# Performance work log

Measured on AMD Instinct MI355X. Metric: run time of the kernel, lower is better.

## Reference

```python
import jax, jax.numpy as jnp
import numpy as np

N = 65536          # nodes per snapshot
B = 32             # batch
COMP = 2           # components (u, v)
SFC = 2            # number of space-filling-curve orderings
K, S, P = 32, 4, 16  # dimension==2 branch: kernel, stride, padding
CHANNELS = [2, 4, 8, 16, 16, 16]  # per-layer channels (x2 until num_final_channels=16)
NCONV = 5          # conv sizes: 65536->16385->4097->1025->257->65
FINAL_SIZE = 65


def _neigh_idx(n):
    # get_neighbourhood_md(arange(n), gen_neighbour_keys(1), ordering=True):
    # per-node [i-1, i, i+1], clamped at boundaries.
    i = jnp.arange(n)
    return jnp.stack([jnp.clip(i - 1, 0, n - 1), i, jnp.clip(i + 1, 0, n - 1)], axis=-1)


def setup_inputs() -> dict:
    key = jax.random.key(0)
    ks = jax.random.split(key, 16)
    d = {}
    d["x"] = jax.random.normal(ks[0], (B, N, COMP), jnp.float32)
    d["orderings"] = jax.random.randint(ks[1], (SFC, N), 0, N)  # SFC permutations (gather indices)
    d["sp_w"] = jnp.ones((N, 3), jnp.float32) / 3.0  # NearestNeighbouring weights (shared over sfcs)
    d["sp_b"] = jnp.zeros((N,), jnp.float32)
    for j in range(NCONV):
        cin, cout = CHANNELS[j], CHANNELS[j + 1]
        d[f"conv_w{j}"] = jax.random.normal(ks[2 + j], (cout, cin, K), jnp.float32) * (1.0 / np.sqrt(cin * K))
        d[f"conv_b{j}"] = jnp.zeros((cout,), jnp.float32)
    fc_in = SFC * CHANNELS[-1] * FINAL_SIZE  # 2080
    d["fc1_w"] = jax.random.normal(ks[8], (128, fc_in), jnp.float32) * (1.0 / np.sqrt(fc_in))
    d["fc1_b"] = jnp.zeros((128,), jnp.float32)
    d["fc2_w"] = jax.random.normal(ks[9], (16, 128), jnp.float32) * (1.0 / np.sqrt(128))
    d["fc2_b"] = jnp.zeros((16,), jnp.float32)
    return d


def _forward(x, orderings, sp_w, sp_b, conv_ws, conv_bs, fc1_w, fc1_b, fc2_w, fc2_b):
    neigh = _neigh_idx(N)  # (N,3)
    feats = []
    for i in range(SFC):
        a = x[:, orderings[i], :]            # SFC permutation gather -> (B,N,C)
        a = jnp.transpose(a, (0, 2, 1))      # (B,C,N)
        g = a[:, :, neigh]                   # neighbourhood gather -> (B,C,N,3)
        a = jnp.tanh(jnp.einsum('bcnk,nk->bcn', g, sp_w) + sp_b)  # sparse NN combine
        for w, b in zip(conv_ws, conv_bs):
            a = jax.lax.conv_general_dilated(a, w, (S,), [(P, P)],
                                             dimension_numbers=('NCH', 'OIH', 'NCH'))
            a = jnp.tanh(a + b[None, :, None])
        feats.append(a.reshape(a.shape[0], -1))  # (B, 16*65)
    h = jnp.concatenate(feats, axis=-1)          # (B, 2080)
    h = jnp.tanh(h @ fc1_w.T + fc1_b)            # (B, 128)
    h = jnp.tanh(h @ fc2_w.T + fc2_b)            # (B, 16) latent
    return h


def reference(x, orderings, sp_w, sp_b, conv_w0, conv_b0, conv_w1, conv_b1, conv_w2, conv_b2,
              conv_w3, conv_b3, conv_w4, conv_b4, fc1_w, fc1_b, fc2_w, fc2_b):
    conv_ws = [conv_w0, conv_w1, conv_w2, conv_w3, conv_w4]
    conv_bs = [conv_b0, conv_b1, conv_b2, conv_b3, conv_b4]
    return _forward(x, orderings, sp_w, sp_b, conv_ws, conv_bs, fc1_w, fc1_b, fc2_w, fc2_b)
```

## Files before the change

### kernel.cpp

```cpp
#include <hip/hip_runtime.h>
#include <math.h>

#define NPTS 65536

__device__ __forceinline__ float4 ld4_guard(const float* __restrict__ row, int pos, int hi) {
    float4 v;
    if (pos >= 0 && pos + 4 <= hi) {
        v = *(const float4*)(row + pos);
    } else {
        v.x = (pos + 0 >= 0 && pos + 0 < hi) ? row[pos + 0] : 0.f;
        v.y = (pos + 1 >= 0 && pos + 1 < hi) ? row[pos + 1] : 0.f;
        v.z = (pos + 2 >= 0 && pos + 2 < hi) ? row[pos + 2] : 0.f;
        v.w = (pos + 3 >= 0 && pos + 3 < hi) ? row[pos + 3] : 0.f;
    }
    return v;
}

__device__ __forceinline__ int pmap(int p) { return p + ((p >> 5) << 2); }

__global__ __launch_bounds__(256) void transpose_kernel(const float* __restrict__ x,
                                                        float* __restrict__ xt)
{
    __shared__ float tile[64][65];
    int n0 = blockIdx.x * 64;
    int tid = threadIdx.x;
    int lane = tid & 63, w = tid >> 6;
    const float2* x2 = (const float2*)x;
#pragma unroll
    for (int bq = 0; bq < 8; ++bq) {
        int b = bq * 4 + w;
        float2 v = x2[(size_t)b * NPTS + n0 + lane];
        tile[lane][b * 2 + 0] = v.x;
        tile[lane][b * 2 + 1] = v.y;
    }
    __syncthreads();
    int f4 = tid & 15;
#pragma unroll
    for (int rq = 0; rq < 4; ++rq) {
        int r = rq * 16 + (tid >> 4);
        float4 v = make_float4(tile[r][f4 * 4 + 0], tile[r][f4 * 4 + 1],
                               tile[r][f4 * 4 + 2], tile[r][f4 * 4 + 3]);
        *(float4*)&xt[(size_t)(n0 + r) * 64 + f4 * 4] = v;
    }
}

__global__ __launch_bounds__(256) void smooth_kernel(const float* __restrict__ xt,
                                                     const int* __restrict__ ord,
                                                     const float* __restrict__ sp_w,
                                                     const float* __restrict__ sp_b,
                                                     float* __restrict__ s)
{
    __shared__ int s_idx[130];
    __shared__ float rows[130][65];
    int n0 = blockIdx.x * 128;
    int tid = threadIdx.x;
    if (tid < 130) {
        int g = n0 - 1 + tid;
        g = g < 0 ? 0 : (g > NPTS - 1 ? NPTS - 1 : g);
        s_idx[tid] = ord[g];
    }
    __syncthreads();
    for (int q = tid; q < 130 * 16; q += 256) {
        int r = q >> 4, f4 = q & 15;
        float4 v = *(const float4*)&xt[(size_t)s_idx[r] * 64 + f4 * 4];
        rows[r][f4 * 4 + 0] = v.x; rows[r][f4 * 4 + 1] = v.y;
        rows[r][f4 * 4 + 2] = v.z; rows[r][f4 * 4 + 3] = v.w;
    }
    __syncthreads();
    int n_local = tid & 127, half = tid >> 7;
    int n = n0 + n_local;
    float w0 = sp_w[n * 3 + 0], w1 = sp_w[n * 3 + 1], w2 = sp_w[n * 3 + 2];
    float bb = sp_b[n];
#pragma unroll 4
    for (int bc = 0; bc < 64; bc += 2) {
        int bce = bc + half;
        float v = w0 * rows[n_local][bce] + w1 * rows[n_local + 1][bce]
                + w2 * rows[n_local + 2][bce] + bb;
        s[(size_t)bce * NPTS + n] = tanhf(v);
    }
}

__global__ __launch_bounds__(256, 2) void conv0_wpc(
    const float* __restrict__ in,
    const float* __restrict__ w,
    const float* __restrict__ bias,
    float* __restrict__ out)
{
    constexpr int SPAN = 2076;
    __shared__ float in_s[2][2336];

    int bid = blockIdx.x;
    int tile = bid % 33;
    int b = bid / 33;
    int tid = threadIdx.x;

    int base = tile * 2048 - 16;
    const float* inb = in + (size_t)b * 2 * NPTS;
    for (int q = tid; q < 2 * (SPAN / 4); q += 256) {
        int ci = q / (SPAN / 4), fp = q - ci * (SPAN / 4);
        int p = 4 * fp;
        float4 v = ld4_guard(inb + (size_t)ci * NPTS, base + p, NPTS);
        *(float4*)&in_s[ci][pmap(p)] = v;
    }
    __syncthreads();

    int lane = tid & 63;
    int co_u = __builtin_amdgcn_readfirstlane(tid >> 6);

    float acc[8];
    float bv = bias[co_u];
#pragma unroll
    for (int j = 0; j < 8; ++j) acc[j] = bv;

#pragma unroll 1
    for (int ci = 0; ci < 2; ++ci) {
        const float* wb = w + (co_u * 2 + ci) * 32;
        float wv[32];
#pragma unroll
        for (int k = 0; k < 32; ++k) wv[k] = wb[k];
        float4 v[15];
#pragma unroll
        for (int k = 0; k < 15; ++k)
            v[k] = *(const float4*)&in_s[ci][pmap(32 * lane + 4 * k)];
#pragma unroll
        for (int k4 = 0; k4 < 8; ++k4) {
            float wx = wv[4 * k4], wy = wv[4 * k4 + 1], wz = wv[4 * k4 + 2], ww = wv[4 * k4 + 3];
#pragma unroll
            for (int j = 0; j < 8; ++j)
                acc[j] += v[j + k4].x * wx + v[j + k4].y * wy
                        + v[j + k4].z * wz + v[j + k4].w * ww;
        }
    }

    int l0 = tile * 512 + lane * 8;
    size_t row = ((size_t)b * 4 + co_u) * 16388;
    if (l0 + 8 <= 16385) {
        float4 s0 = make_float4(tanhf(acc[0]), tanhf(acc[1]), tanhf(acc[2]), tanhf(acc[3]));
        float4 s1 = make_float4(tanhf(acc[4]), tanhf(acc[5]), tanhf(acc[6]), tanhf(acc[7]));
        *(float4*)&out[row + l0] = s0;
        *(float4*)&out[row + l0 + 4] = s1;
    } else {
#pragma unroll
        for (int j = 0; j < 8; ++j)
            if (l0 + j < 16385) out[row + l0 + j] = tanhf(acc[j]);
    }
}

__global__ __launch_bounds__(512) void conv1_wpc(
    const float* __restrict__ in,
    const float* __restrict__ w,
    const float* __restrict__ bias,
    float* __restrict__ out)
{
    constexpr int SPAN = 1052;
    __shared__ float in_s[4][1184];

    int bid = blockIdx.x;
    int tile = bid % 17;
    int b = bid / 17;
    int tid = threadIdx.x;

    int base = tile * 1024 - 16;
    const float* inb = in + (size_t)b * 4 * 16388;
    for (int q = tid; q < 4 * (SPAN / 4); q += 512) {
        int ci = q / (SPAN / 4), fp = q - ci * (SPAN / 4);
        int p = 4 * fp;
        float4 v = ld4_guard(inb + (size_t)ci * 16388, base + p, 16385);
        *(float4*)&in_s[ci][pmap(p)] = v;
    }
    __syncthreads();

    int lane = tid & 63;
    int co_u = __builtin_amdgcn_readfirstlane(tid >> 6);

    float acc[4];
    float bv = bias[co_u];
#pragma unroll
    for (int j = 0; j < 4; ++j) acc[j] = bv;

#pragma unroll 1
    for (int ci = 0; ci < 4; ++ci) {
        const float* wb = w + (co_u * 4 + ci) * 32;
        float wv[32];
#pragma unroll
        for (int k = 0; k < 32; ++k) wv[k] = wb[k];
        float4 v[11];
#pragma unroll
        for (int k = 0; k < 11; ++k)
            v[k] = *(const float4*)&in_s[ci][pmap(16 * lane + 4 * k)];
#pragma unroll
        for (int k4 = 0; k4 < 8; ++k4) {
            float wx = wv[4 * k4], wy = wv[4 * k4 + 1], wz = wv[4 * k4 + 2], ww = wv[4 * k4 + 3];
#pragma unroll
            for (int j = 0; j < 4; ++j)
                acc[j] += v[j + k4].x * wx + v[j + k4].y * wy
                        + v[j + k4].z * wz + v[j + k4].w * ww;
        }
    }

    int l0 = tile * 256 + lane * 4;
    size_t row = ((size_t)b * 8 + co_u) * 4100;
    if (l0 + 4 <= 4097) {
        float4 s0 = make_float4(tanhf(acc[0]), tanhf(acc[1]), tanhf(acc[2]), tanhf(acc[3]));
        *(float4*)&out[row + l0] = s0;
    } else {
#pragma unroll
        for (int j = 0; j < 4; ++j)
            if (l0 + j < 4097) out[row + l0 + j] = tanhf(acc[j]);
    }
}

__global__ __launch_bounds__(512) void conv2_wpc(
    const float* __restrict__ in,
    const float* __restrict__ w,
    const float* __restrict__ bias,
    float* __restrict__ out)
{
    constexpr int SPAN = 540;
    __shared__ float in_s[8][608];

    int bid = blockIdx.x;
    int tile = bid % 9;
    int b = bid / 9;
    int tid = threadIdx.x;

    int base = tile * 512 - 16;
    const float* inb = in + (size_t)b * 8 * 4100;
    for (int q = tid; q < 8 * (SPAN / 4); q += 512) {
        int ci = q / (SPAN / 4), fp = q - ci * (SPAN / 4);
        int p = 4 * fp;
        float4 v = ld4_guard(inb + (size_t)ci * 4100, base + p, 4097);
        *(float4*)&in_s[ci][pmap(p)] = v;
    }
    __syncthreads();

    int lane = tid & 63;
    int co_u = __builtin_amdgcn_readfirstlane(tid >> 6);

    float acc[2][2];
    acc[0][0] = acc[0][1] = bias[co_u];
    acc[1][0] = acc[1][1] = bias[co_u + 8];

#pragma unroll 1
    for (int ci = 0; ci < 8; ++ci) {
        const float* wa = w + (size_t)(co_u * 8 + ci) * 32;
        const float* wb = w + (size_t)((co_u + 8) * 8 + ci) * 32;
        float4 v[9];
#pragma unroll
        for (int k = 0; k < 9; ++k)
            v[k] = *(const float4*)&in_s[ci][pmap(8 * lane + 4 * k)];
#pragma unroll
        for (int k4 = 0; k4 < 8; ++k4) {
            float4 wva = *(const float4*)(wa + 4 * k4);
            float4 wvb = *(const float4*)(wb + 4 * k4);
#pragma unroll
            for (int j = 0; j < 2; ++j) {
                acc[0][j] += v[k4 + j].x * wva.x + v[k4 + j].y * wva.y
                           + v[k4 + j].z * wva.z + v[k4 + j].w * wva.w;
                acc[1][j] += v[k4 + j].x * wvb.x + v[k4 + j].y * wvb.y
                           + v[k4 + j].z * wvb.z + v[k4 + j].w * wvb.w;
            }
        }
    }

    int l0 = tile * 128 + lane * 2;
#pragma unroll
    for (int h = 0; h < 2; ++h) {
        size_t row = ((size_t)b * 16 + co_u + 8 * h) * 1028;
        if (l0 + 2 <= 1025) {
            float2 st2 = make_float2(tanhf(acc[h][0]), tanhf(acc[h][1]));
            *(float2*)&out[row + l0] = st2;
        } else {
#pragma unroll
            for (int j = 0; j < 2; ++j)
                if (l0 + j < 1025) out[row + l0 + j] = tanhf(acc[h][j]);
        }
    }
}

__global__ __launch_bounds__(512) void conv3_wpc(
    const float* __restrict__ in,
    const float* __restrict__ w,
    const float* __restrict__ bias,
    float* __restrict__ out)
{
    constexpr int SPAN = 284;
    __shared__ float in_s[16][320];

    int bid = blockIdx.x;
    int tile = bid % 5;
    int b = bid / 5;
    int tid = threadIdx.x;

    int base = tile * 256 - 16;
    const float* inb = in + (size_t)b * 16 * 1028;
    for (int q = tid; q < 16 * (SPAN / 4); q += 512) {
        int ci = q / (SPAN / 4), fp = q - ci * (SPAN / 4);
        int p = 4 * fp;
        float4 v = ld4_guard(inb + (size_t)ci * 1028, base + p, 1025);
        *(float4*)&in_s[ci][pmap(p)] = v;
    }
    __syncthreads();

    int lane = tid & 63;
    int co_u = __builtin_amdgcn_readfirstlane(tid >> 6);

    float acc0 = bias[co_u], acc1 = bias[co_u + 8];

#pragma unroll 1
    for (int ci = 0; ci < 16; ++ci) {
        const float* wa = w + (size_t)(co_u * 16 + ci) * 32;
        const float* wb = w + (size_t)((co_u + 8) * 16 + ci) * 32;
        float4 v[8];
#pragma unroll
        for (int k = 0; k < 8; ++k)
            v[k] = *(const float4*)&in_s[ci][pmap(4 * lane + 4 * k)];
#pragma unroll
        for (int k4 = 0; k4 < 8; ++k4) {
            float4 wva = *(const float4*)(wa + 4 * k4);
            float4 wvb = *(const float4*)(wb + 4 * k4);
            acc0 += v[k4].x * wva.x + v[k4].y * wva.y
                  + v[k4].z * wva.z + v[k4].w * wva.w;
            acc1 += v[k4].x * wvb.x + v[k4].y * wvb.y
                  + v[k4].z * wvb.z + v[k4].w * wvb.w;
        }
    }

    int l3 = tile * 64 + lane;
    if (l3 < 257) {
        out[((size_t)b * 16 + co_u) * 260 + l3] = tanhf(acc0);
        out[((size_t)b * 16 + co_u + 8) * 260 + l3] = tanhf(acc1);
    }
}

__global__ __launch_bounds__(256) void conv4_kernel(
    const float* __restrict__ c3,
    const float* __restrict__ w4, const float* __restrict__ b4,
    float* __restrict__ feats, int ibase)
{
    __shared__ __align__(16) float st[16][320];
    __shared__ float w4s[8][16][32];
    int b = blockIdx.x >> 1, h = blockIdx.x & 1;
    int tid = threadIdx.x;
    for (int i = tid; i < 8 * 16 * 32; i += 256) ((float*)w4s)[i] = w4[h * 4096 + i];
    const float* c3b = c3 + (size_t)b * 16 * 260;
    for (int q = tid; q < 16 * 72; q += 256) {
        int ci = q / 72, p4 = q - ci * 72;
        float4 v = ld4_guard(c3b + (size_t)ci * 260, 4 * p4 - 16, 257);
        *(float4*)&st[ci][pmap(4 * p4)] = v;
    }
    __syncthreads();
    for (int q = tid; q < 520; q += 256) {
        int co_l = q / 65, l4 = q - co_l * 65;
        int co = h * 8 + co_l;
        float acc = b4[co];
#pragma unroll 1
        for (int ci = 0; ci < 16; ++ci) {
#pragma unroll
            for (int k4 = 0; k4 < 8; ++k4) {
                float4 v = *(const float4*)&st[ci][pmap(4 * l4 + 4 * k4)];
                const float* wk = &w4s[co_l][ci][4 * k4];
                acc += v.x * wk[0] + v.y * wk[1] + v.z * wk[2] + v.w * wk[3];
            }
        }
        feats[(size_t)(b & 31) * 2080 + (size_t)((b >> 5) + ibase) * 1040 + co * 65 + l4]
            = tanhf(acc);
    }
}

__global__ __launch_bounds__(256) void fc1_kernel(const float* __restrict__ h,
                                                  const float* __restrict__ w,
                                                  const float* __restrict__ bias,
                                                  float* __restrict__ out)
{
    int lane = threadIdx.x & 63;
    int wid = blockIdx.x * 4 + (threadIdx.x >> 6);
#pragma unroll
    for (int r = 0; r < 4; ++r) {
        int o = wid + r * 1024;
        int b = o >> 7, j = o & 127;
        const float4* h4 = (const float4*)(h + (size_t)b * 2080);
        const float4* w4 = (const float4*)(w + (size_t)j * 2080);
        float acc = 0.f;
#pragma unroll
        for (int q = 0; q < 8; ++q) {
            float4 a = h4[lane + 64 * q], c = w4[lane + 64 * q];
            acc += a.x * c.x + a.y * c.y + a.z * c.z + a.w * c.w;
        }
        if (lane < 8) {
            float4 a = h4[512 + lane], c = w4[512 + lane];
            acc += a.x * c.x + a.y * c.y + a.z * c.z + a.w * c.w;
        }
        for (int off = 32; off; off >>= 1) acc += __shfl_down(acc, off, 64);
        if (lane == 0) out[b * 128 + j] = tanhf(acc + bias[j]);
    }
}

__global__ __launch_bounds__(256) void fc2_kernel(const float* __restrict__ h,
                                                  const float* __restrict__ w,
                                                  const float* __restrict__ bias,
                                                  float* __restrict__ out)
{
    int lane = threadIdx.x & 63;
    int o = blockIdx.x * 4 + (threadIdx.x >> 6);
    int b = o >> 4, j = o & 15;
    const float* hb = h + (size_t)b * 128;
    const float* wj = w + (size_t)j * 128;
    float acc = hb[lane] * wj[lane] + hb[lane + 64] * wj[lane + 64];
    for (int off = 32; off; off >>= 1) acc += __shfl_down(acc, off, 64);
    if (lane == 0) out[o] = tanhf(acc + bias[j]);
}

extern "C" void kernel_launch(void* const* d_in, const int* in_sizes, int n_in,
                              void* d_out, int out_size, void* d_ws, size_t ws_size,
                              hipStream_t stream)
{
    const float* x = (const float*)d_in[0];
    const int* orderings = (const int*)d_in[1];
    const float* sp_w = (const float*)d_in[2];
    const float* sp_b = (const float*)d_in[3];
    const float* conv_w[5];
    const float* conv_b[5];
    for (int j = 0; j < 5; ++j) {
        conv_w[j] = (const float*)d_in[4 + 2 * j];
        conv_b[j] = (const float*)d_in[5 + 2 * j];
    }
    const float* fc1_w = (const float*)d_in[14];
    const float* fc1_b = (const float*)d_in[15];
    const float* fc2_w = (const float*)d_in[16];
    const float* fc2_b = (const float*)d_in[17];

    float* ws = (float*)d_ws;

    if (ws_size >= 12583936ull * 4ull) {
        size_t o_xt = 0, o_c0 = 0, o_s = 4195328;
        size_t o_c1 = 4195328, o_c2 = 6294528, o_c3 = 7347200;
        size_t o_f = 7613440, o_h1 = 7680000;

        transpose_kernel<<<NPTS / 64, 256, 0, stream>>>(x, ws + o_xt);
        smooth_kernel<<<512, 256, 0, stream>>>(ws + o_xt, orderings, sp_w, sp_b, ws + o_s);
        smooth_kernel<<<512, 256, 0, stream>>>(ws + o_xt, orderings + NPTS, sp_w, sp_b,
                                               ws + o_s + 4194304);

        conv0_wpc<<<64 * 33, 256, 0, stream>>>(ws + o_s, conv_w[0], conv_b[0], ws + o_c0);
        conv1_wpc<<<64 * 17, 512, 0, stream>>>(ws + o_c0, conv_w[1], conv_b[1], ws + o_c1);
        conv2_wpc<<<64 * 9, 512, 0, stream>>>(ws + o_c1, conv_w[2], conv_b[2], ws + o_c2);
        conv3_wpc<<<64 * 5, 512, 0, stream>>>(ws + o_c2, conv_w[3], conv_b[3], ws + o_c3);
        conv4_kernel<<<128, 256, 0, stream>>>(ws + o_c3, conv_w[4], conv_b[4],
                                              ws + o_f, 0);
        fc1_kernel<<<256, 256, 0, stream>>>(ws + o_f, fc1_w, fc1_b, ws + o_h1);
        fc2_kernel<<<128, 256, 0, stream>>>(ws + o_h1, fc2_w, fc2_b, (float*)d_out);
    } else {
        size_t o_xt = 0, o_s = 4194304, o_c0 = 8388608;
        size_t o_c1 = 4194304, o_c2 = 5243904, o_c3 = 5770240;
        size_t o_f = 10486272, o_h1 = 10552832;

        transpose_kernel<<<NPTS / 64, 256, 0, stream>>>(x, ws + o_xt);
        for (int i = 0; i < 2; ++i) {
            smooth_kernel<<<512, 256, 0, stream>>>(ws + o_xt, orderings + (size_t)i * NPTS,
                                                   sp_w, sp_b, ws + o_s);
            conv0_wpc<<<32 * 33, 256, 0, stream>>>(ws + o_s, conv_w[0], conv_b[0], ws + o_c0);
            conv1_wpc<<<32 * 17, 512, 0, stream>>>(ws + o_c0, conv_w[1], conv_b[1], ws + o_c1);
            conv2_wpc<<<32 * 9, 512, 0, stream>>>(ws + o_c1, conv_w[2], conv_b[2], ws + o_c2);
            conv3_wpc<<<32 * 5, 512, 0, stream>>>(ws + o_c2, conv_w[3], conv_b[3], ws + o_c3);
            conv4_kernel<<<64, 256, 0, stream>>>(ws + o_c3, conv_w[4], conv_b[4],
                                                 ws + o_f, i);
        }
        fc1_kernel<<<256, 256, 0, stream>>>(ws + o_f, fc1_w, fc1_b, ws + o_h1);
        fc2_kernel<<<128, 256, 0, stream>>>(ws + o_h1, fc2_w, fc2_b, (float*)d_out);
    }
}
```

Baseline: 138.7 us.

## Merge smooth launches, fuse fc1/fc2, halve conv1-3 blocks with more outputs per thread

The two per-ordering smooth launches become one launch that picks the ordering from the block index. fc1 and fc2 become a single per-batch kernel that keeps the hidden layer in shared memory. conv1–conv3 now run 256-thread blocks where each wave computes two or four output channels, so each LDS input load is reused across more channels. The aims are fewer launches and less shared-memory traffic per FLOP. The cost is more registers per thread, and the fused FC uses only 32 blocks, which leaves little parallelism for the 2080-wide fc1 reduction.

```diff
diff --git a/kernel.cpp b/kernel.cpp
--- a/kernel.cpp
+++ b/kernel.cpp
@@ -44,15 +44,20 @@
     }
 }
 
-__global__ __launch_bounds__(256) void smooth_kernel(const float* __restrict__ xt,
-                                                     const int* __restrict__ ord,
-                                                     const float* __restrict__ sp_w,
-                                                     const float* __restrict__ sp_b,
-                                                     float* __restrict__ s)
+__global__ __launch_bounds__(256) void smooth2_kernel(const float* __restrict__ xt,
+                                                      const int* __restrict__ ord0,
+                                                      const float* __restrict__ sp_w,
+                                                      const float* __restrict__ sp_b,
+                                                      float* __restrict__ s0)
 {
     __shared__ int s_idx[130];
     __shared__ float rows[130][65];
-    int n0 = blockIdx.x * 128;
+    int bid = blockIdx.x;
+    int i = bid >> 9;
+    int t = bid & 511;
+    const int* ord = ord0 + (size_t)i * NPTS;
+    float* s = s0 + (size_t)i * 4194304;
+    int n0 = t * 128;
     int tid = threadIdx.x;
     if (tid < 130) {
         int g = n0 - 1 + tid;
@@ -146,7 +151,7 @@
     }
 }
 
-__global__ __launch_bounds__(512) void conv1_wpc(
+__global__ __launch_bounds__(256, 2) void conv1_wpc(
     const float* __restrict__ in,
     const float* __restrict__ w,
     const float* __restrict__ bias,
@@ -162,7 +167,7 @@
 
     int base = tile * 1024 - 16;
     const float* inb = in + (size_t)b * 4 * 16388;
-    for (int q = tid; q < 4 * (SPAN / 4); q += 512) {
+    for (int q = tid; q < 4 * (SPAN / 4); q += 256) {
         int ci = q / (SPAN / 4), fp = q - ci * (SPAN / 4);
         int p = 4 * fp;
         float4 v = ld4_guard(inb + (size_t)ci * 16388, base + p, 16385);
@@ -173,88 +178,25 @@
     int lane = tid & 63;
     int co_u = __builtin_amdgcn_readfirstlane(tid >> 6);
 
-    float acc[4];
-    float bv = bias[co_u];
-#pragma unroll
-    for (int j = 0; j < 4; ++j) acc[j] = bv;
+    float acc[2][4];
+    float b0 = bias[co_u], b1v = bias[co_u + 4];
+#pragma unroll
+    for (int j = 0; j < 4; ++j) { acc[0][j] = b0; acc[1][j] = b1v; }
 
 #pragma unroll 1
     for (int ci = 0; ci < 4; ++ci) {
-        const float* wb = w + (co_u * 4 + ci) * 32;
-        float wv[32];
-#pragma unroll
-        for (int k = 0; k < 32; ++k) wv[k] = wb[k];
+        const float* wa = w + (size_t)(co_u * 4 + ci) * 32;
+        const float* wb = w + (size_t)((co_u + 4) * 4 + ci) * 32;
         float4 v[11];
 #pragma unroll
         for (int k = 0; k < 11; ++k)
             v[k] = *(const float4*)&in_s[ci][pmap(16 * lane + 4 * k)];
-#pragma unroll
-        for (int k4 = 0; k4 < 8; ++k4) {
-            float wx = wv[4 * k4], wy = wv[4 * k4 + 1], wz = wv[4 * k4 + 2], ww = wv[4 * k4 + 3];
-#pragma unroll
-            for (int j = 0; j < 4; ++j)
-                acc[j] += v[j + k4].x * wx + v[j + k4].y * wy
-                        + v[j + k4].z * wz + v[j + k4].w * ww;
-        }
-    }
-
-    int l0 = tile * 256 + lane * 4;
-    size_t row = ((size_t)b * 8 + co_u) * 4100;
-    if (l0 + 4 <= 4097) {
-        float4 s0 = make_float4(tanhf(acc[0]), tanhf(acc[1]), tanhf(acc[2]), tanhf(acc[3]));
-        *(float4*)&out[row + l0] = s0;
-    } else {
-#pragma unroll
-        for (int j = 0; j < 4; ++j)
-            if (l0 + j < 4097) out[row + l0 + j] = tanhf(acc[j]);
-    }
-}
-
-__global__ __launch_bounds__(512) void conv2_wpc(
-    const float* __restrict__ in,
-    const float* __restrict__ w,
-    const float* __restrict__ bias,
-    float* __restrict__ out)
-{
-    constexpr int SPAN = 540;
-    __shared__ float in_s[8][608];
-
-    int bid = blockIdx.x;
-    int tile = bid % 9;
-    int b = bid / 9;
-    int tid = threadIdx.x;
-
-    int base = tile * 512 - 16;
-    const float* inb = in + (size_t)b * 8 * 4100;
-    for (int q = tid; q < 8 * (SPAN / 4); q += 512) {
-        int ci = q / (SPAN / 4), fp = q - ci * (SPAN / 4);
-        int p = 4 * fp;
-        float4 v = ld4_guard(inb + (size_t)ci * 4100, base + p, 4097);
-        *(float4*)&in_s[ci][pmap(p)] = v;
-    }
-    __syncthreads();
-
-    int lane = tid & 63;
-    int co_u = __builtin_amdgcn_readfirstlane(tid >> 6);
-
-    float acc[2][2];
-    acc[0][0] = acc[0][1] = bias[co_u];
-    acc[1][0] = acc[1][1] = bias[co_u + 8];
-
-#pragma unroll 1
-    for (int ci = 0; ci < 8; ++ci) {
-        const float* wa = w + (size_t)(co_u * 8 + ci) * 32;
-        const float* wb = w + (size_t)((co_u + 8) * 8 + ci) * 32;
-        float4 v[9];
-#pragma unroll
-        for (int k = 0; k < 9; ++k)
-            v[k] = *(const float4*)&in_s[ci][pmap(8 * lane + 4 * k)];
 #pragma unroll
         for (int k4 = 0; k4 < 8; ++k4) {
             float4 wva = *(const float4*)(wa + 4 * k4);
             float4 wvb = *(const float4*)(wb + 4 * k4);
 #pragma unroll
-            for (int j = 0; j < 2; ++j) {
+            for (int j = 0; j < 4; ++j) {
                 acc[0][j] += v[k4 + j].x * wva.x + v[k4 + j].y * wva.y
                            + v[k4 + j].z * wva.z + v[k4 + j].w * wva.w;
                 acc[1][j] += v[k4 + j].x * wvb.x + v[k4 + j].y * wvb.y
@@ -263,27 +205,96 @@
         }
     }
 
-    int l0 = tile * 128 + lane * 2;
+    int l0 = tile * 256 + lane * 4;
 #pragma unroll
     for (int h = 0; h < 2; ++h) {
-        size_t row = ((size_t)b * 16 + co_u + 8 * h) * 1028;
-        if (l0 + 2 <= 1025) {
-            float2 st2 = make_float2(tanhf(acc[h][0]), tanhf(acc[h][1]));
-            *(float2*)&out[row + l0] = st2;
+        size_t row = ((size_t)b * 8 + co_u + 4 * h) * 4100;
+        if (l0 + 4 <= 4097) {
+            float4 s0 = make_float4(tanhf(acc[h][0]), tanhf(acc[h][1]),
+                                    tanhf(acc[h][2]), tanhf(acc[h][3]));
+            *(float4*)&out[row + l0] = s0;
         } else {
 #pragma unroll
-            for (int j = 0; j < 2; ++j)
-                if (l0 + j < 1025) out[row + l0 + j] = tanhf(acc[h][j]);
-        }
-    }
-}
-
-__global__ __launch_bounds__(512) void conv3_wpc(
+            for (int j = 0; j < 4; ++j)
+                if (l0 + j < 4097) out[row + l0 + j] = tanhf(acc[h][j]);
+        }
+    }
+}
+
+__global__ __launch_bounds__(256, 2) void conv2_wpc(
     const float* __restrict__ in,
     const float* __restrict__ w,
     const float* __restrict__ bias,
     float* __restrict__ out)
 {
+    constexpr int SPAN = 540;
+    __shared__ float in_s[8][608];
+
+    int bid = blockIdx.x;
+    int tile = bid % 9;
+    int b = bid / 9;
+    int tid = threadIdx.x;
+
+    int base = tile * 512 - 16;
+    const float* inb = in + (size_t)b * 8 * 4100;
+    for (int q = tid; q < 8 * (SPAN / 4); q += 256) {
+        int ci = q / (SPAN / 4), fp = q - ci * (SPAN / 4);
+        int p = 4 * fp;
+        float4 v = ld4_guard(inb + (size_t)ci * 4100, base + p, 4097);
+        *(float4*)&in_s[ci][pmap(p)] = v;
+    }
+    __syncthreads();
+
+    int lane = tid & 63;
+    int co_u = __builtin_amdgcn_readfirstlane(tid >> 6);
+
+    float acc[4][2];
+#pragma unroll
+    for (int c = 0; c < 4; ++c) {
+        float bv = bias[co_u + 4 * c];
+        acc[c][0] = bv; acc[c][1] = bv;
+    }
+
+#pragma unroll 1
+    for (int ci = 0; ci < 8; ++ci) {
+        float4 v[9];
+#pragma unroll
+        for (int k = 0; k < 9; ++k)
+            v[k] = *(const float4*)&in_s[ci][pmap(8 * lane + 4 * k)];
+#pragma unroll
+        for (int k4 = 0; k4 < 8; ++k4) {
+#pragma unroll
+            for (int c = 0; c < 4; ++c) {
+                float4 wv = *(const float4*)(w + (size_t)((co_u + 4 * c) * 8 + ci) * 32 + 4 * k4);
+#pragma unroll
+                for (int j = 0; j < 2; ++j)
+                    acc[c][j] += v[k4 + j].x * wv.x + v[k4 + j].y * wv.y
+                               + v[k4 + j].z * wv.z + v[k4 + j].w * wv.w;
+            }
+        }
+    }
+
+    int l0 = tile * 128 + lane * 2;
+#pragma unroll
+    for (int c = 0; c < 4; ++c) {
+        size_t row = ((size_t)b * 16 + co_u + 4 * c) * 1028;
+        if (l0 + 2 <= 1025) {
+            float2 st2 = make_float2(tanhf(acc[c][0]), tanhf(acc[c][1]));
+            *(float2*)&out[row + l0] = st2;
+        } else {
+#pragma unroll
+            for (int j = 0; j < 2; ++j)
+                if (l0 + j < 1025) out[row + l0 + j] = tanhf(acc[c][j]);
+        }
+    }
+}
+
+__global__ __launch_bounds__(256, 2) void conv3_wpc(
+    const float* __restrict__ in,
+    const float* __restrict__ w,
+    const float* __restrict__ bias,
+    float* __restrict__ out)
+{
     constexpr int SPAN = 284;
     __shared__ float in_s[16][320];
 
@@ -294,7 +305,7 @@
 
     int base = tile * 256 - 16;
     const float* inb = in + (size_t)b * 16 * 1028;
-    for (int q = tid; q < 16 * (SPAN / 4); q += 512) {
+    for (int q = tid; q < 16 * (SPAN / 4); q += 256) {
         int ci = q / (SPAN / 4), fp = q - ci * (SPAN / 4);
         int p = 4 * fp;
         float4 v = ld4_guard(inb + (size_t)ci * 1028, base + p, 1025);
@@ -305,31 +316,32 @@
     int lane = tid & 63;
     int co_u = __builtin_amdgcn_readfirstlane(tid >> 6);
 
-    float acc0 = bias[co_u], acc1 = bias[co_u + 8];
+    float acc[4];
+#pragma unroll
+    for (int c = 0; c < 4; ++c) acc[c] = bias[co_u + 4 * c];
 
 #pragma unroll 1
     for (int ci = 0; ci < 16; ++ci) {
-        const float* wa = w + (size_t)(co_u * 16 + ci) * 32;
-        const float* wb = w + (size_t)((co_u + 8) * 16 + ci) * 32;
         float4 v[8];
 #pragma unroll
         for (int k = 0; k < 8; ++k)
             v[k] = *(const float4*)&in_s[ci][pmap(4 * lane + 4 * k)];
 #pragma unroll
         for (int k4 = 0; k4 < 8; ++k4) {
-            float4 wva = *(const float4*)(wa + 4 * k4);
-            float4 wvb = *(const float4*)(wb + 4 * k4);
-            acc0 += v[k4].x * wva.x + v[k4].y * wva.y
-                  + v[k4].z * wva.z + v[k4].w * wva.w;
-            acc1 += v[k4].x * wvb.x + v[k4].y * wvb.y
-                  + v[k4].z * wvb.z + v[k4].w * wvb.w;
+#pragma unroll
+            for (int c = 0; c < 4; ++c) {
+                float4 wv = *(const float4*)(w + (size_t)((co_u + 4 * c) * 16 + ci) * 32 + 4 * k4);
+                acc[c] += v[k4].x * wv.x + v[k4].y * wv.y
+                        + v[k4].z * wv.z + v[k4].w * wv.w;
+            }
         }
     }
 
     int l3 = tile * 64 + lane;
     if (l3 < 257) {
-        out[((size_t)b * 16 + co_u) * 260 + l3] = tanhf(acc0);
-        out[((size_t)b * 16 + co_u + 8) * 260 + l3] = tanhf(acc1);
+#pragma unroll
+        for (int c = 0; c < 4; ++c)
+            out[((size_t)b * 16 + co_u + 4 * c) * 260 + l3] = tanhf(acc[c]);
     }
 }
 
@@ -368,19 +380,22 @@
     }
 }
 
-__global__ __launch_bounds__(256) void fc1_kernel(const float* __restrict__ h,
-                                                  const float* __restrict__ w,
-                                                  const float* __restrict__ bias,
-                                                  float* __restrict__ out)
-{
-    int lane = threadIdx.x & 63;
-    int wid = blockIdx.x * 4 + (threadIdx.x >> 6);
-#pragma unroll
-    for (int r = 0; r < 4; ++r) {
-        int o = wid + r * 1024;
-        int b = o >> 7, j = o & 127;
-        const float4* h4 = (const float4*)(h + (size_t)b * 2080);
-        const float4* w4 = (const float4*)(w + (size_t)j * 2080);
+__global__ __launch_bounds__(512) void fc12_kernel(const float* __restrict__ feats,
+                                                   const float* __restrict__ w1,
+                                                   const float* __restrict__ b1,
+                                                   const float* __restrict__ w2,
+                                                   const float* __restrict__ b2,
+                                                   float* __restrict__ out)
+{
+    __shared__ float h1s[128];
+    int b = blockIdx.x;
+    int tid = threadIdx.x, lane = tid & 63, w = tid >> 6;
+    const float4* h4 = (const float4*)(feats + (size_t)b * 2080);
+
+#pragma unroll 1
+    for (int jj = 0; jj < 16; ++jj) {
+        int j = w * 16 + jj;
+        const float4* w4 = (const float4*)(w1 + (size_t)j * 2080);
         float acc = 0.f;
 #pragma unroll
         for (int q = 0; q < 8; ++q) {
@@ -392,23 +407,18 @@
             acc += a.x * c.x + a.y * c.y + a.z * c.z + a.w * c.w;
         }
         for (int off = 32; off; off >>= 1) acc += __shfl_down(acc, off, 64);
-        if (lane == 0) out[b * 128 + j] = tanhf(acc + bias[j]);
-    }
-}
-
-__global__ __launch_bounds__(256) void fc2_kernel(const float* __restrict__ h,
-                                                  const float* __restrict__ w,
-                                                  const float* __restrict__ bias,
-                                                  float* __restrict__ out)
-{
-    int lane = threadIdx.x & 63;
-    int o = blockIdx.x * 4 + (threadIdx.x >> 6);
-    int b = o >> 4, j = o & 15;
-    const float* hb = h + (size_t)b * 128;
-    const float* wj = w + (size_t)j * 128;
-    float acc = hb[lane] * wj[lane] + hb[lane + 64] * wj[lane + 64];
-    for (int off = 32; off; off >>= 1) acc += __shfl_down(acc, off, 64);
-    if (lane == 0) out[o] = tanhf(acc + bias[j]);
+        if (lane == 0) h1s[j] = tanhf(acc + b1[j]);
+    }
+    __syncthreads();
+
+#pragma unroll
+    for (int r = 0; r < 2; ++r) {
+        int j2 = w * 2 + r;
+        const float* wj = w2 + (size_t)j2 * 128;
+        float acc = h1s[lane] * wj[lane] + h1s[lane + 64] * wj[lane + 64];
+        for (int off = 32; off; off >>= 1) acc += __shfl_down(acc, off, 64);
+        if (lane == 0) out[b * 16 + j2] = tanhf(acc + b2[j2]);
+    }
 }
 
 extern "C" void kernel_launch(void* const* d_in, const int* in_sizes, int n_in,
@@ -434,39 +444,36 @@
 
     if (ws_size >= 12583936ull * 4ull) {
         size_t o_xt = 0, o_c0 = 0, o_s = 4195328;
-        size_t o_c1 = 4195328, o_c2 = 6294528, o_c3 = 7347200;
-        size_t o_f = 7613440, o_h1 = 7680000;
+        size_t o_c1 = 4195328, o_c2 = 6294528, o_c3 = 7347200, o_f = 7613440;
 
         transpose_kernel<<<NPTS / 64, 256, 0, stream>>>(x, ws + o_xt);
-        smooth_kernel<<<512, 256, 0, stream>>>(ws + o_xt, orderings, sp_w, sp_b, ws + o_s);
-        smooth_kernel<<<512, 256, 0, stream>>>(ws + o_xt, orderings + NPTS, sp_w, sp_b,
-                                               ws + o_s + 4194304);
-
+        smooth2_kernel<<<1024, 256, 0, stream>>>(ws + o_xt, orderings, sp_w, sp_b,
+                                                 ws + o_s);
         conv0_wpc<<<64 * 33, 256, 0, stream>>>(ws + o_s, conv_w[0], conv_b[0], ws + o_c0);
-        conv1_wpc<<<64 * 17, 512, 0, stream>>>(ws + o_c0, conv_w[1], conv_b[1], ws + o_c1);
-        conv2_wpc<<<64 * 9, 512, 0, stream>>>(ws + o_c1, conv_w[2], conv_b[2], ws + o_c2);
-        conv3_wpc<<<64 * 5, 512, 0, stream>>>(ws + o_c2, conv_w[3], conv_b[3], ws + o_c3);
+        conv1_wpc<<<64 * 17, 256, 0, stream>>>(ws + o_c0, conv_w[1], conv_b[1], ws + o_c1);
+        conv2_wpc<<<64 * 9, 256, 0, stream>>>(ws + o_c1, conv_w[2], conv_b[2], ws + o_c2);
+        conv3_wpc<<<64 * 5, 256, 0, stream>>>(ws + o_c2, conv_w[3], conv_b[3], ws + o_c3);
         conv4_kernel<<<128, 256, 0, stream>>>(ws + o_c3, conv_w[4], conv_b[4],
                                               ws + o_f, 0);
-        fc1_kernel<<<256, 256, 0, stream>>>(ws + o_f, fc1_w, fc1_b, ws + o_h1);
-        fc2_kernel<<<128, 256, 0, stream>>>(ws + o_h1, fc2_w, fc2_b, (float*)d_out);
+        fc12_kernel<<<32, 512, 0, stream>>>(ws + o_f, fc1_w, fc1_b, fc2_w, fc2_b,
+                                            (float*)d_out);
     } else {
         size_t o_xt = 0, o_s = 4194304, o_c0 = 8388608;
-        size_t o_c1 = 4194304, o_c2 = 5243904, o_c3 = 5770240;
-        size_t o_f = 10486272, o_h1 = 10552832;
+        size_t o_c1 = 4194304, o_c2 = 5243904, o_c3 = 5770240, o_f = 10486272;
 
         transpose_kernel<<<NPTS / 64, 256, 0, stream>>>(x, ws + o_xt);
         for (int i = 0; i < 2; ++i) {
-            smooth_kernel<<<512, 256, 0, stream>>>(ws + o_xt, orderings + (size_t)i * NPTS,
-                                                   sp_w, sp_b, ws + o_s);
+            smooth2_kernel<<<512, 256, 0, stream>>>(ws + o_xt,
+                                                    orderings + (size_t)i * NPTS,
+                                                    sp_w, sp_b, ws + o_s);
             conv0_wpc<<<32 * 33, 256, 0, stream>>>(ws + o_s, conv_w[0], conv_b[0], ws + o_c0);
-            conv1_wpc<<<32 * 17, 512, 0, stream>>>(ws + o_c0, conv_w[1], conv_b[1], ws + o_c1);
-            conv2_wpc<<<32 * 9, 512, 0, stream>>>(ws + o_c1, conv_w[2], conv_b[2], ws + o_c2);
-            conv3_wpc<<<32 * 5, 512, 0, stream>>>(ws + o_c2, conv_w[3], conv_b[3], ws + o_c3);
+            conv1_wpc<<<32 * 17, 256, 0, stream>>>(ws + o_c0, conv_w[1], conv_b[1], ws + o_c1);
+            conv2_wpc<<<32 * 9, 256, 0, stream>>>(ws + o_c1, conv_w[2], conv_b[2], ws + o_c2);
+            conv3_wpc<<<32 * 5, 256, 0, stream>>>(ws + o_c2, conv_w[3], conv_b[3], ws + o_c3);
             conv4_kernel<<<64, 256, 0, stream>>>(ws + o_c3, conv_w[4], conv_b[4],
                                                  ws + o_f, i);
         }
-        fc1_kernel<<<256, 256, 0, stream>>>(ws + o_f, fc1_w, fc1_b, ws + o_h1);
-        fc2_kernel<<<128, 256, 0, stream>>>(ws + o_h1, fc2_w, fc2_b, (float*)d_out);
-    }
-}
+        fc12_kernel<<<32, 512, 0, stream>>>(ws + o_f, fc1_w, fc1_b, fc2_w, fc2_b,
+                                            (float*)d_out);
+    }
+}
```

New measurement: 146.6 us. +5.7%, slower.
